# Kernel optimization log

Hardware: AMD Instinct MI355X
Metric: run time of the kernel (lower is better)

The kernel has to match this reference:

```python
import jax, jax.numpy as jnp
import numpy as np

N = 50000
E = 800000
D_IN, D_HID, D_OUT = 256, 512, 256
LN_EPS = 1e-5


def setup_inputs() -> dict:
    key = jax.random.key(0)
    ks = jax.random.split(key, 8)
    return {
        "v": jax.random.normal(ks[0], (N, D_IN), dtype=jnp.float32),
        "edge_weight": jax.random.uniform(ks[1], (E,), dtype=jnp.float32),
        "epsilon": jnp.zeros((1, 1), dtype=jnp.float32),
        "w1": jax.random.normal(ks[2], (D_HID, D_IN), dtype=jnp.float32) * (1.0 / np.sqrt(D_IN)),
        "b1": jnp.zeros((D_HID,), dtype=jnp.float32),
        "g1": jnp.ones((D_HID,), dtype=jnp.float32),
        "beta1": jnp.zeros((D_HID,), dtype=jnp.float32),
        "w2": jax.random.normal(ks[3], (D_OUT, D_HID), dtype=jnp.float32) * (1.0 / np.sqrt(D_HID)),
        "b2": jnp.zeros((D_OUT,), dtype=jnp.float32),
        "g2": jnp.ones((D_OUT,), dtype=jnp.float32),
        "beta2": jnp.zeros((D_OUT,), dtype=jnp.float32),
        "src": jax.random.randint(ks[4], (E,), 0, N, dtype=jnp.int32),
        "dst": jax.random.randint(ks[5], (E,), 0, N, dtype=jnp.int32),
    }


def _layer_norm(x, g, b):
    mu = jnp.mean(x, axis=-1, keepdims=True)
    var = jnp.mean(jnp.square(x - mu), axis=-1, keepdims=True)
    return (x - mu) * jax.lax.rsqrt(var + LN_EPS) * g + b


def reference(v, edge_weight, epsilon, w1, b1, g1, beta1, w2, b2, g2, beta2, src, dst):
    # sparse adjacency aggregation: agg[dst] += w * v[src]   (torch.sparse.mm(a, v))
    msgs = v[src] * edge_weight[:, None]            # [E, D_IN]
    agg = jax.ops.segment_sum(msgs, dst, num_segments=v.shape[0])  # [N, D_IN]
    h = agg + epsilon * v                            # epsilon residual
    # MLP: Linear -> LayerNorm -> ReLU  (x2)
    h = jax.nn.relu(_layer_norm(h @ w1.T + b1, g1, beta1))
    h = jax.nn.relu(_layer_norm(h @ w2.T + b2, g2, beta2))
    return h
```

## Files before the change

kernel.cpp:

```cpp
#include <hip/hip_runtime.h>

#define D_IN 256
#define D_HID 512
#define D_OUT 256
#define LN_EPS 1e-5f
#define SCAN_B 512

typedef __attribute__((ext_vector_type(8))) short bf16x8;
typedef __attribute__((ext_vector_type(4))) float f32x4;

__device__ __forceinline__ ushort f2bf(float x) {
    union { float f; unsigned u; } c; c.f = x;
    unsigned r = c.u + 0x7FFFu + ((c.u >> 16) & 1u);
    return (ushort)(r >> 16);
}
__device__ __forceinline__ float bf2f(unsigned b) {
    union { unsigned u; float f; } c; c.u = b << 16;
    return c.f;
}

__global__ void zero_kernel(int* __restrict__ p, int n) {
    int i = blockIdx.x * 256 + threadIdx.x;
    if (i < n) p[i] = 0;
}

__global__ void hist_kernel(const int* __restrict__ dst, int* __restrict__ cnt, int E) {
    int e = blockIdx.x * 256 + threadIdx.x;
    if (e < E) atomicAdd(&cnt[dst[e]], 1);
}

__global__ __launch_bounds__(SCAN_B) void scan1_kernel(const int* __restrict__ cnt,
                                                       int* __restrict__ offs,
                                                       int* __restrict__ bsum, int n) {
    __shared__ int s[SCAN_B];
    int i = blockIdx.x * SCAN_B + threadIdx.x;
    int x = (i < n) ? cnt[i] : 0;
    s[threadIdx.x] = x;
    __syncthreads();
    for (int o = 1; o < SCAN_B; o <<= 1) {
        int t = (threadIdx.x >= (unsigned)o) ? s[threadIdx.x - o] : 0;
        __syncthreads();
        s[threadIdx.x] += t;
        __syncthreads();
    }
    if (i < n) offs[i] = s[threadIdx.x] - x;
    if (threadIdx.x == SCAN_B - 1) bsum[blockIdx.x] = s[threadIdx.x];
}

__global__ __launch_bounds__(128) void scan2_kernel(int* __restrict__ bsum, int nb) {
    __shared__ int s[128];
    int x = (threadIdx.x < (unsigned)nb) ? bsum[threadIdx.x] : 0;
    s[threadIdx.x] = x;
    __syncthreads();
    for (int o = 1; o < 128; o <<= 1) {
        int t = (threadIdx.x >= (unsigned)o) ? s[threadIdx.x - o] : 0;
        __syncthreads();
        s[threadIdx.x] += t;
        __syncthreads();
    }
    if (threadIdx.x < (unsigned)nb) bsum[threadIdx.x] = s[threadIdx.x] - x;
}

__global__ __launch_bounds__(SCAN_B) void scan3_kernel(int* __restrict__ offs,
                                                       int* __restrict__ cursor,
                                                       const int* __restrict__ bsum,
                                                       int n, int E) {
    int i = blockIdx.x * SCAN_B + threadIdx.x;
    if (i < n) {
        int v0 = offs[i] + bsum[blockIdx.x];
        offs[i] = v0;
        cursor[i] = v0;
    }
    if (i == 0) offs[n] = E;
}

__global__ void fill_kernel(const int* __restrict__ src, const int* __restrict__ dst,
                            const float* __restrict__ ew, int* __restrict__ cursor,
                            int2* __restrict__ perm, int E) {
    int e = blockIdx.x * 256 + threadIdx.x;
    if (e >= E) return;
    int p = atomicAdd(&cursor[dst[e]], 1);
    perm[p] = make_int2(src[e], __float_as_int(ew[e]));
}

__global__ void cvt_bf16_kernel(const float* __restrict__ in, ushort* __restrict__ out, int n4) {
    int i = blockIdx.x * 256 + threadIdx.x;
    if (i >= n4) return;
    float4 x = ((const float4*)in)[i];
    ((ushort4*)out)[i] = make_ushort4(f2bf(x.x), f2bf(x.y), f2bf(x.z), f2bf(x.w));
}

__global__ void cvt_w_kernel(const float* __restrict__ w1, const float* __restrict__ w2,
                             ushort* __restrict__ w1b, ushort* __restrict__ w2b) {
    int i = blockIdx.x * 256 + threadIdx.x;
    const float* src; ushort* dst; int j;
    if (i < 32768) { src = w1; dst = w1b; j = i; }
    else           { src = w2; dst = w2b; j = i - 32768; }
    float4 x = ((const float4*)src)[j];
    ((ushort4*)dst)[j] = make_ushort4(f2bf(x.x), f2bf(x.y), f2bf(x.z), f2bf(x.w));
}

__global__ __launch_bounds__(256) void aggregate_kernel(
    const ushort* __restrict__ vb, const float* __restrict__ eps_p,
    const int* __restrict__ offs, const int2* __restrict__ perm,
    ushort* __restrict__ aggb, int N) {
    int node = blockIdx.x * 4 + (threadIdx.x >> 6);
    if (node >= N) return;
    int lane = threadIdx.x & 63;
    int beg = offs[node], end = offs[node + 1];
    float a0 = 0.f, a1 = 0.f, a2 = 0.f, a3 = 0.f;

    int i = beg;
    for (; i + 4 <= end; i += 4) {
        int2 p0 = perm[i + 0], p1 = perm[i + 1], p2 = perm[i + 2], p3 = perm[i + 3];
        float w0 = __int_as_float(p0.y), w1 = __int_as_float(p1.y);
        float w2 = __int_as_float(p2.y), w3 = __int_as_float(p3.y);
        ushort4 r0 = ((const ushort4*)(vb + (size_t)p0.x * D_IN))[lane];
        ushort4 r1 = ((const ushort4*)(vb + (size_t)p1.x * D_IN))[lane];
        ushort4 r2 = ((const ushort4*)(vb + (size_t)p2.x * D_IN))[lane];
        ushort4 r3 = ((const ushort4*)(vb + (size_t)p3.x * D_IN))[lane];
        a0 += w0 * bf2f(r0.x) + w1 * bf2f(r1.x) + w2 * bf2f(r2.x) + w3 * bf2f(r3.x);
        a1 += w0 * bf2f(r0.y) + w1 * bf2f(r1.y) + w2 * bf2f(r2.y) + w3 * bf2f(r3.y);
        a2 += w0 * bf2f(r0.z) + w1 * bf2f(r1.z) + w2 * bf2f(r2.z) + w3 * bf2f(r3.z);
        a3 += w0 * bf2f(r0.w) + w1 * bf2f(r1.w) + w2 * bf2f(r2.w) + w3 * bf2f(r3.w);
    }
    for (; i < end; ++i) {
        int2 p = perm[i];
        float w = __int_as_float(p.y);
        ushort4 r = ((const ushort4*)(vb + (size_t)p.x * D_IN))[lane];
        a0 += w * bf2f(r.x); a1 += w * bf2f(r.y);
        a2 += w * bf2f(r.z); a3 += w * bf2f(r.w);
    }
    float eps = eps_p[0];
    ushort4 m = ((const ushort4*)(vb + (size_t)node * D_IN))[lane];
    a0 += eps * bf2f(m.x); a1 += eps * bf2f(m.y);
    a2 += eps * bf2f(m.z); a3 += eps * bf2f(m.w);
    ((ushort4*)(aggb + (size_t)node * D_IN))[lane] =
        make_ushort4(f2bf(a0), f2bf(a1), f2bf(a2), f2bf(a3));
}

template <int COLS, int WRITE_BF16>
__global__ __launch_bounds__(256) void gemm_ln_kernel(
    const ushort* __restrict__ A, const ushort* __restrict__ B,
    const float* __restrict__ bias, const float* __restrict__ g,
    const float* __restrict__ beta, void* __restrict__ Cv, int M, int K) {
    constexpr int CW = COLS / 4;
    constexpr int CF = CW / 16;
    __shared__ ushort As[32 * 32];
    __shared__ ushort Bs[COLS * 32];
    __shared__ float red[2][32][4];
    __shared__ float mu_s[32], rs_s[32];

    int t = threadIdx.x;
    int w = t >> 6, lane = t & 63;
    int row0 = blockIdx.x * 32;
    int fr = lane & 15, q = lane >> 4, kb = q * 8;
    int lrow = lane >> 2;
    int lcol = (lane & 3) * 8;

    f32x4 acc[2][CF];
    #pragma unroll
    for (int i = 0; i < 2; ++i)
        #pragma unroll
        for (int c = 0; c < CF; ++c) {
            f32x4 z = {0.f, 0.f, 0.f, 0.f};
            acc[i][c] = z;
        }

    for (int k0 = 0; k0 < K; k0 += 32) {
        #pragma unroll
        for (int c = 0; c < CF; ++c) {
            int br = w * CW + c * 16 + lrow;
            const ushort* gp = B + (size_t)br * K + k0 + lcol;
            __builtin_amdgcn_global_load_lds(
                (const __attribute__((address_space(1))) void*)gp,
                (__attribute__((address_space(3))) void*)(&Bs[(w * CW + c * 16) * 32]),
                16, 0, 0);
        }
        if (w < 2) {
            int ar = row0 + w * 16 + lrow;
            if (ar > M - 1) ar = M - 1;
            const ushort* gp = A + (size_t)ar * K + k0 + lcol;
            __builtin_amdgcn_global_load_lds(
                (const __attribute__((address_space(1))) void*)gp,
                (__attribute__((address_space(3))) void*)(&As[(w * 16) * 32]),
                16, 0, 0);
        }
        __syncthreads();

        bf16x8 af[2], bf[CF];
        af[0] = *(const bf16x8*)&As[fr * 32 + kb];
        af[1] = *(const bf16x8*)&As[(16 + fr) * 32 + kb];
        #pragma unroll
        for (int c = 0; c < CF; ++c)
            bf[c] = *(const bf16x8*)&Bs[(w * CW + c * 16 + fr) * 32 + kb];
        #pragma unroll
        for (int i = 0; i < 2; ++i)
            #pragma unroll
            for (int c = 0; c < CF; ++c)
                acc[i][c] = __builtin_amdgcn_mfma_f32_16x16x32_bf16(af[i], bf[c], acc[i][c], 0, 0, 0);
        __syncthreads();
    }

    float bi[CF], gg[CF], bb[CF];
    #pragma unroll
    for (int c = 0; c < CF; ++c) {
        int col = w * CW + c * 16 + fr;
        bi[c] = bias[col]; gg[c] = g[col]; bb[c] = beta[col];
    }

    #pragma unroll
    for (int i = 0; i < 2; ++i) {
        #pragma unroll
        for (int r = 0; r < 4; ++r) {
            float s = 0.f, sq = 0.f;
            #pragma unroll
            for (int c = 0; c < CF; ++c) {
                float x = acc[i][c][r] + bi[c];
                acc[i][c][r] = x;
                s += x; sq += x * x;
            }
            #pragma unroll
            for (int o = 1; o < 16; o <<= 1) {
                s  += __shfl_xor(s, o, 64);
                sq += __shfl_xor(sq, o, 64);
            }
            if (fr == 0) {
                int row = i * 16 + q * 4 + r;
                red[0][row][w] = s;
                red[1][row][w] = sq;
            }
        }
    }
    __syncthreads();
    if (t < 32) {
        float s  = red[0][t][0] + red[0][t][1] + red[0][t][2] + red[0][t][3];
        float sq = red[1][t][0] + red[1][t][1] + red[1][t][2] + red[1][t][3];
        float mu = s / (float)COLS;
        float var = sq / (float)COLS - mu * mu;
        mu_s[t] = mu;
        rs_s[t] = rsqrtf(var + LN_EPS);
    }
    __syncthreads();

    #pragma unroll
    for (int i = 0; i < 2; ++i) {
        #pragma unroll
        for (int r = 0; r < 4; ++r) {
            int row = i * 16 + q * 4 + r;
            int grow = row0 + row;
            if (grow >= M) continue;
            float mu = mu_s[row], rs = rs_s[row];
            #pragma unroll
            for (int c = 0; c < CF; ++c) {
                int col = w * CW + c * 16 + fr;
                float y = (acc[i][c][r] - mu) * rs * gg[c] + bb[c];
                y = fmaxf(y, 0.f);
                if (WRITE_BF16)
                    ((ushort*)Cv)[(size_t)grow * COLS + col] = f2bf(y);
                else
                    ((float*)Cv)[(size_t)grow * COLS + col] = y;
            }
        }
    }
}

extern "C" void kernel_launch(void* const* d_in, const int* in_sizes, int n_in,
                              void* d_out, int out_size, void* d_ws, size_t ws_size,
                              hipStream_t stream) {
    const float* v     = (const float*)d_in[0];
    const float* ew    = (const float*)d_in[1];
    const float* eps   = (const float*)d_in[2];
    const float* w1    = (const float*)d_in[3];
    const float* b1    = (const float*)d_in[4];
    const float* g1    = (const float*)d_in[5];
    const float* beta1 = (const float*)d_in[6];
    const float* w2    = (const float*)d_in[7];
    const float* b2    = (const float*)d_in[8];
    const float* g2    = (const float*)d_in[9];
    const float* beta2 = (const float*)d_in[10];
    const int*   src   = (const int*)d_in[11];
    const int*   dst   = (const int*)d_in[12];

    int N = in_sizes[0] / D_IN;
    int E = in_sizes[1];

    float* out = (float*)d_out;

    char* ws = (char*)d_ws;
    size_t off = 0;
    ushort* vb   = (ushort*)(ws + off); off += (size_t)N * D_IN * 2;
    ushort* aggb = (ushort*)(ws + off); off += (size_t)N * D_IN * 2;
    ushort* h1b  = (ushort*)(ws + off); off += (size_t)N * D_HID * 2;
    ushort* w1b  = (ushort*)(ws + off); off += (size_t)D_HID * D_IN * 2;
    ushort* w2b  = (ushort*)(ws + off); off += (size_t)D_OUT * D_HID * 2;
    int* offs     = (int*)(ws + off); off += (size_t)(N + 256) * 4;
    int* cursor   = (int*)(ws + off); off += (size_t)(N + 256) * 4;
    int* bsum     = (int*)(ws + off); off += 1024;
    int2* perm    = (int2*)(ws + off); off += (size_t)E * 8;

    int nb = (N + SCAN_B - 1) / SCAN_B;

    zero_kernel<<<(N + 255) / 256, 256, 0, stream>>>(cursor, N);
    hist_kernel<<<(E + 255) / 256, 256, 0, stream>>>(dst, cursor, E);
    scan1_kernel<<<nb, SCAN_B, 0, stream>>>(cursor, offs, bsum, N);
    scan2_kernel<<<1, 128, 0, stream>>>(bsum, nb);
    scan3_kernel<<<nb, SCAN_B, 0, stream>>>(offs, cursor, bsum, N, E);
    fill_kernel<<<(E + 255) / 256, 256, 0, stream>>>(src, dst, ew, cursor, perm, E);

    cvt_bf16_kernel<<<((size_t)N * D_IN / 4 + 255) / 256, 256, 0, stream>>>(v, vb, N * D_IN / 4);
    cvt_w_kernel<<<256, 256, 0, stream>>>(w1, w2, w1b, w2b);

    aggregate_kernel<<<(N + 3) / 4, 256, 0, stream>>>(vb, eps, offs, perm, aggb, N);

    int mblocks = (N + 31) / 32;
    gemm_ln_kernel<D_HID, 1><<<mblocks, 256, 0, stream>>>(
        aggb, w1b, b1, g1, beta1, h1b, N, D_IN);

    gemm_ln_kernel<D_OUT, 0><<<mblocks, 256, 0, stream>>>(
        h1b, w2b, b2, g2, beta2, out, N, D_HID);
}
```

Before: 363.7 us.

## Fuse aggregation and both GEMM+LayerNorm layers into one kernel, merge prep launches

New measurement: 421.7 us. 1.16x slower.

```diff
diff --git a/kernel.cpp b/kernel.cpp
--- a/kernel.cpp
+++ b/kernel.cpp
@@ -19,9 +19,32 @@
     return c.f;
 }
 
-__global__ void zero_kernel(int* __restrict__ p, int n) {
-    int i = blockIdx.x * 256 + threadIdx.x;
-    if (i < n) p[i] = 0;
+__global__ void prep_kernel(const float* __restrict__ v, const float* __restrict__ w1,
+                            const float* __restrict__ w2, ushort* __restrict__ vb,
+                            ushort* __restrict__ w1b, ushort* __restrict__ w2b,
+                            int* __restrict__ cnt, int n4v, int nzero,
+                            int bv, int bw) {
+    int b = blockIdx.x, t = threadIdx.x;
+    if (b < bv) {
+        int i = b * 256 + t;
+        if (i < n4v) {
+            float4 x = ((const float4*)v)[i];
+            ((ushort4*)vb)[i] = make_ushort4(f2bf(x.x), f2bf(x.y), f2bf(x.z), f2bf(x.w));
+        }
+    } else if (b < bv + bw) {
+        int j = (b - bv) * 256 + t;
+        if (j < 32768) {
+            float4 x = ((const float4*)w1)[j];
+            ((ushort4*)w1b)[j] = make_ushort4(f2bf(x.x), f2bf(x.y), f2bf(x.z), f2bf(x.w));
+        } else {
+            int k = j - 32768;
+            float4 x = ((const float4*)w2)[k];
+            ((ushort4*)w2b)[k] = make_ushort4(f2bf(x.x), f2bf(x.y), f2bf(x.z), f2bf(x.w));
+        }
+    } else {
+        int i = (b - bv - bw) * 256 + t;
+        if (i < nzero) cnt[i] = 0;
+    }
 }
 
 __global__ void hist_kernel(const int* __restrict__ dst, int* __restrict__ cnt, int E) {
@@ -47,27 +70,22 @@
     if (threadIdx.x == SCAN_B - 1) bsum[blockIdx.x] = s[threadIdx.x];
 }
 
-__global__ __launch_bounds__(128) void scan2_kernel(int* __restrict__ bsum, int nb) {
-    __shared__ int s[128];
-    int x = (threadIdx.x < (unsigned)nb) ? bsum[threadIdx.x] : 0;
-    s[threadIdx.x] = x;
-    __syncthreads();
-    for (int o = 1; o < 128; o <<= 1) {
-        int t = (threadIdx.x >= (unsigned)o) ? s[threadIdx.x - o] : 0;
-        __syncthreads();
-        s[threadIdx.x] += t;
-        __syncthreads();
-    }
-    if (threadIdx.x < (unsigned)nb) bsum[threadIdx.x] = s[threadIdx.x] - x;
-}
-
 __global__ __launch_bounds__(SCAN_B) void scan3_kernel(int* __restrict__ offs,
                                                        int* __restrict__ cursor,
                                                        const int* __restrict__ bsum,
-                                                       int n, int E) {
-    int i = blockIdx.x * SCAN_B + threadIdx.x;
+                                                       int n, int E, int nb) {
+    __shared__ int s[SCAN_B];
+    int t = threadIdx.x;
+    s[t] = (t < nb && t < (int)blockIdx.x) ? bsum[t] : 0;
+    __syncthreads();
+    for (int o = SCAN_B / 2; o > 0; o >>= 1) {
+        if (t < o) s[t] += s[t + o];
+        __syncthreads();
+    }
+    int base = s[0];
+    int i = blockIdx.x * SCAN_B + t;
     if (i < n) {
-        int v0 = offs[i] + bsum[blockIdx.x];
+        int v0 = offs[i] + base;
         offs[i] = v0;
         cursor[i] = v0;
     }
@@ -83,71 +101,19 @@
     perm[p] = make_int2(src[e], __float_as_int(ew[e]));
 }
 
-__global__ void cvt_bf16_kernel(const float* __restrict__ in, ushort* __restrict__ out, int n4) {
-    int i = blockIdx.x * 256 + threadIdx.x;
-    if (i >= n4) return;
-    float4 x = ((const float4*)in)[i];
-    ((ushort4*)out)[i] = make_ushort4(f2bf(x.x), f2bf(x.y), f2bf(x.z), f2bf(x.w));
-}
-
-__global__ void cvt_w_kernel(const float* __restrict__ w1, const float* __restrict__ w2,
-                             ushort* __restrict__ w1b, ushort* __restrict__ w2b) {
-    int i = blockIdx.x * 256 + threadIdx.x;
-    const float* src; ushort* dst; int j;
-    if (i < 32768) { src = w1; dst = w1b; j = i; }
-    else           { src = w2; dst = w2b; j = i - 32768; }
-    float4 x = ((const float4*)src)[j];
-    ((ushort4*)dst)[j] = make_ushort4(f2bf(x.x), f2bf(x.y), f2bf(x.z), f2bf(x.w));
-}
-
-__global__ __launch_bounds__(256) void aggregate_kernel(
+#define ASTR 264
+#define HSTR 520
+#define BS1_OFF 8448
+#define BS2_OFF 16640
+
+__global__ __launch_bounds__(256) void mega_kernel(
     const ushort* __restrict__ vb, const float* __restrict__ eps_p,
     const int* __restrict__ offs, const int2* __restrict__ perm,
-    ushort* __restrict__ aggb, int N) {
-    int node = blockIdx.x * 4 + (threadIdx.x >> 6);
-    if (node >= N) return;
-    int lane = threadIdx.x & 63;
-    int beg = offs[node], end = offs[node + 1];
-    float a0 = 0.f, a1 = 0.f, a2 = 0.f, a3 = 0.f;
-
-    int i = beg;
-    for (; i + 4 <= end; i += 4) {
-        int2 p0 = perm[i + 0], p1 = perm[i + 1], p2 = perm[i + 2], p3 = perm[i + 3];
-        float w0 = __int_as_float(p0.y), w1 = __int_as_float(p1.y);
-        float w2 = __int_as_float(p2.y), w3 = __int_as_float(p3.y);
-        ushort4 r0 = ((const ushort4*)(vb + (size_t)p0.x * D_IN))[lane];
-        ushort4 r1 = ((const ushort4*)(vb + (size_t)p1.x * D_IN))[lane];
-        ushort4 r2 = ((const ushort4*)(vb + (size_t)p2.x * D_IN))[lane];
-        ushort4 r3 = ((const ushort4*)(vb + (size_t)p3.x * D_IN))[lane];
-        a0 += w0 * bf2f(r0.x) + w1 * bf2f(r1.x) + w2 * bf2f(r2.x) + w3 * bf2f(r3.x);
-        a1 += w0 * bf2f(r0.y) + w1 * bf2f(r1.y) + w2 * bf2f(r2.y) + w3 * bf2f(r3.y);
-        a2 += w0 * bf2f(r0.z) + w1 * bf2f(r1.z) + w2 * bf2f(r2.z) + w3 * bf2f(r3.z);
-        a3 += w0 * bf2f(r0.w) + w1 * bf2f(r1.w) + w2 * bf2f(r2.w) + w3 * bf2f(r3.w);
-    }
-    for (; i < end; ++i) {
-        int2 p = perm[i];
-        float w = __int_as_float(p.y);
-        ushort4 r = ((const ushort4*)(vb + (size_t)p.x * D_IN))[lane];
-        a0 += w * bf2f(r.x); a1 += w * bf2f(r.y);
-        a2 += w * bf2f(r.z); a3 += w * bf2f(r.w);
-    }
-    float eps = eps_p[0];
-    ushort4 m = ((const ushort4*)(vb + (size_t)node * D_IN))[lane];
-    a0 += eps * bf2f(m.x); a1 += eps * bf2f(m.y);
-    a2 += eps * bf2f(m.z); a3 += eps * bf2f(m.w);
-    ((ushort4*)(aggb + (size_t)node * D_IN))[lane] =
-        make_ushort4(f2bf(a0), f2bf(a1), f2bf(a2), f2bf(a3));
-}
-
-template <int COLS, int WRITE_BF16>
-__global__ __launch_bounds__(256) void gemm_ln_kernel(
-    const ushort* __restrict__ A, const ushort* __restrict__ B,
-    const float* __restrict__ bias, const float* __restrict__ g,
-    const float* __restrict__ beta, void* __restrict__ Cv, int M, int K) {
-    constexpr int CW = COLS / 4;
-    constexpr int CF = CW / 16;
-    __shared__ ushort As[32 * 32];
-    __shared__ ushort Bs[COLS * 32];
+    const ushort* __restrict__ w1b, const ushort* __restrict__ w2b,
+    const float* __restrict__ b1, const float* __restrict__ g1, const float* __restrict__ be1,
+    const float* __restrict__ b2, const float* __restrict__ g2, const float* __restrict__ be2,
+    float* __restrict__ out, int N) {
+    __shared__ ushort lds[24832];
     __shared__ float red[2][32][4];
     __shared__ float mu_s[32], rs_s[32];
 
@@ -155,111 +121,226 @@
     int w = t >> 6, lane = t & 63;
     int row0 = blockIdx.x * 32;
     int fr = lane & 15, q = lane >> 4, kb = q * 8;
-    int lrow = lane >> 2;
-    int lcol = (lane & 3) * 8;
-
-    f32x4 acc[2][CF];
+    int lrow = lane >> 2, lcol = (lane & 3) * 8;
+
+    float epsv = eps_p[0];
+    for (int s = 0; s < 8; ++s) {
+        int lnode = w * 8 + s;
+        int node = row0 + lnode;
+        float a0 = 0.f, a1 = 0.f, a2 = 0.f, a3 = 0.f;
+        if (node < N) {
+            int beg = offs[node], end = offs[node + 1];
+            int i = beg;
+            for (; i + 4 <= end; i += 4) {
+                int2 p0 = perm[i + 0], p1 = perm[i + 1], p2 = perm[i + 2], p3 = perm[i + 3];
+                float w0 = __int_as_float(p0.y), w1f = __int_as_float(p1.y);
+                float w2f = __int_as_float(p2.y), w3 = __int_as_float(p3.y);
+                ushort4 r0 = ((const ushort4*)(vb + (size_t)p0.x * D_IN))[lane];
+                ushort4 r1 = ((const ushort4*)(vb + (size_t)p1.x * D_IN))[lane];
+                ushort4 r2 = ((const ushort4*)(vb + (size_t)p2.x * D_IN))[lane];
+                ushort4 r3 = ((const ushort4*)(vb + (size_t)p3.x * D_IN))[lane];
+                a0 += w0 * bf2f(r0.x) + w1f * bf2f(r1.x) + w2f * bf2f(r2.x) + w3 * bf2f(r3.x);
+                a1 += w0 * bf2f(r0.y) + w1f * bf2f(r1.y) + w2f * bf2f(r2.y) + w3 * bf2f(r3.y);
+                a2 += w0 * bf2f(r0.z) + w1f * bf2f(r1.z) + w2f * bf2f(r2.z) + w3 * bf2f(r3.z);
+                a3 += w0 * bf2f(r0.w) + w1f * bf2f(r1.w) + w2f * bf2f(r2.w) + w3 * bf2f(r3.w);
+            }
+            for (; i < end; ++i) {
+                int2 p = perm[i];
+                float wf = __int_as_float(p.y);
+                ushort4 r = ((const ushort4*)(vb + (size_t)p.x * D_IN))[lane];
+                a0 += wf * bf2f(r.x); a1 += wf * bf2f(r.y);
+                a2 += wf * bf2f(r.z); a3 += wf * bf2f(r.w);
+            }
+            ushort4 m = ((const ushort4*)(vb + (size_t)node * D_IN))[lane];
+            a0 += epsv * bf2f(m.x); a1 += epsv * bf2f(m.y);
+            a2 += epsv * bf2f(m.z); a3 += epsv * bf2f(m.w);
+        }
+        uint2 pk;
+        pk.x = (unsigned)f2bf(a0) | ((unsigned)f2bf(a1) << 16);
+        pk.y = (unsigned)f2bf(a2) | ((unsigned)f2bf(a3) << 16);
+        *(uint2*)&lds[lnode * ASTR + lane * 4] = pk;
+    }
+    __syncthreads();
+
+    f32x4 acc[2][8];
     #pragma unroll
     for (int i = 0; i < 2; ++i)
         #pragma unroll
-        for (int c = 0; c < CF; ++c) {
+        for (int c = 0; c < 8; ++c) {
             f32x4 z = {0.f, 0.f, 0.f, 0.f};
             acc[i][c] = z;
         }
 
-    for (int k0 = 0; k0 < K; k0 += 32) {
-        #pragma unroll
-        for (int c = 0; c < CF; ++c) {
-            int br = w * CW + c * 16 + lrow;
-            const ushort* gp = B + (size_t)br * K + k0 + lcol;
+    for (int k0 = 0; k0 < D_IN; k0 += 32) {
+        #pragma unroll
+        for (int c = 0; c < 8; ++c) {
+            int br = w * 128 + c * 16 + lrow;
+            const ushort* gp = w1b + (size_t)br * D_IN + k0 + lcol;
             __builtin_amdgcn_global_load_lds(
                 (const __attribute__((address_space(1))) void*)gp,
-                (__attribute__((address_space(3))) void*)(&Bs[(w * CW + c * 16) * 32]),
+                (__attribute__((address_space(3))) void*)(&lds[BS1_OFF + (w * 128 + c * 16) * 32]),
                 16, 0, 0);
         }
-        if (w < 2) {
-            int ar = row0 + w * 16 + lrow;
-            if (ar > M - 1) ar = M - 1;
-            const ushort* gp = A + (size_t)ar * K + k0 + lcol;
+        __syncthreads();
+        bf16x8 af[2], bf[8];
+        af[0] = *(const bf16x8*)&lds[fr * ASTR + k0 + kb];
+        af[1] = *(const bf16x8*)&lds[(16 + fr) * ASTR + k0 + kb];
+        #pragma unroll
+        for (int c = 0; c < 8; ++c)
+            bf[c] = *(const bf16x8*)&lds[BS1_OFF + (w * 128 + c * 16 + fr) * 32 + kb];
+        #pragma unroll
+        for (int i = 0; i < 2; ++i)
+            #pragma unroll
+            for (int c = 0; c < 8; ++c)
+                acc[i][c] = __builtin_amdgcn_mfma_f32_16x16x32_bf16(af[i], bf[c], acc[i][c], 0, 0, 0);
+        __syncthreads();
+    }
+
+    {
+        float bi[8], gg[8], bb[8];
+        #pragma unroll
+        for (int c = 0; c < 8; ++c) {
+            int col = w * 128 + c * 16 + fr;
+            bi[c] = b1[col]; gg[c] = g1[col]; bb[c] = be1[col];
+        }
+        #pragma unroll
+        for (int i = 0; i < 2; ++i) {
+            #pragma unroll
+            for (int r = 0; r < 4; ++r) {
+                float s = 0.f, sq = 0.f;
+                #pragma unroll
+                for (int c = 0; c < 8; ++c) {
+                    float x = acc[i][c][r] + bi[c];
+                    acc[i][c][r] = x;
+                    s += x; sq += x * x;
+                }
+                #pragma unroll
+                for (int o = 1; o < 16; o <<= 1) {
+                    s  += __shfl_xor(s, o, 64);
+                    sq += __shfl_xor(sq, o, 64);
+                }
+                if (fr == 0) {
+                    int row = i * 16 + q * 4 + r;
+                    red[0][row][w] = s;
+                    red[1][row][w] = sq;
+                }
+            }
+        }
+        __syncthreads();
+        if (t < 32) {
+            float s  = red[0][t][0] + red[0][t][1] + red[0][t][2] + red[0][t][3];
+            float sq = red[1][t][0] + red[1][t][1] + red[1][t][2] + red[1][t][3];
+            float mu = s / (float)D_HID;
+            float var = sq / (float)D_HID - mu * mu;
+            mu_s[t] = mu;
+            rs_s[t] = rsqrtf(var + LN_EPS);
+        }
+        __syncthreads();
+        #pragma unroll
+        for (int i = 0; i < 2; ++i) {
+            #pragma unroll
+            for (int r = 0; r < 4; ++r) {
+                int row = i * 16 + q * 4 + r;
+                float mu = mu_s[row], rs = rs_s[row];
+                #pragma unroll
+                for (int c = 0; c < 8; ++c) {
+                    int col = w * 128 + c * 16 + fr;
+                    float y = (acc[i][c][r] - mu) * rs * gg[c] + bb[c];
+                    lds[row * HSTR + col] = f2bf(fmaxf(y, 0.f));
+                }
+            }
+        }
+    }
+    __syncthreads();
+
+    f32x4 acc2[2][4];
+    #pragma unroll
+    for (int i = 0; i < 2; ++i)
+        #pragma unroll
+        for (int c = 0; c < 4; ++c) {
+            f32x4 z = {0.f, 0.f, 0.f, 0.f};
+            acc2[i][c] = z;
+        }
+
+    for (int k0 = 0; k0 < D_HID; k0 += 32) {
+        #pragma unroll
+        for (int c = 0; c < 4; ++c) {
+            int br = w * 64 + c * 16 + lrow;
+            const ushort* gp = w2b + (size_t)br * D_HID + k0 + lcol;
             __builtin_amdgcn_global_load_lds(
                 (const __attribute__((address_space(1))) void*)gp,
-                (__attribute__((address_space(3))) void*)(&As[(w * 16) * 32]),
+                (__attribute__((address_space(3))) void*)(&lds[BS2_OFF + (w * 64 + c * 16) * 32]),
                 16, 0, 0);
         }
         __syncthreads();
-
-        bf16x8 af[2], bf[CF];
-        af[0] = *(const bf16x8*)&As[fr * 32 + kb];
-        af[1] = *(const bf16x8*)&As[(16 + fr) * 32 + kb];
-        #pragma unroll
-        for (int c = 0; c < CF; ++c)
-            bf[c] = *(const bf16x8*)&Bs[(w * CW + c * 16 + fr) * 32 + kb];
+        bf16x8 af[2], bf[4];
+        af[0] = *(const bf16x8*)&lds[fr * HSTR + k0 + kb];
+        af[1] = *(const bf16x8*)&lds[(16 + fr) * HSTR + k0 + kb];
+        #pragma unroll
+        for (int c = 0; c < 4; ++c)
+            bf[c] = *(const bf16x8*)&lds[BS2_OFF + (w * 64 + c * 16 + fr) * 32 + kb];
         #pragma unroll
         for (int i = 0; i < 2; ++i)
             #pragma unroll
-            for (int c = 0; c < CF; ++c)
-                acc[i][c] = __builtin_amdgcn_mfma_f32_16x16x32_bf16(af[i], bf[c], acc[i][c], 0, 0, 0);
-        __syncthreads();
-    }
-
-    float bi[CF], gg[CF], bb[CF];
-    #pragma unroll
-    for (int c = 0; c < CF; ++c) {
-        int col = w * CW + c * 16 + fr;
-        bi[c] = bias[col]; gg[c] = g[col]; bb[c] = beta[col];
-    }
-
-    #pragma unroll
-    for (int i = 0; i < 2; ++i) {
-        #pragma unroll
-        for (int r = 0; r < 4; ++r) {
-            float s = 0.f, sq = 0.f;
-            #pragma unroll
-            for (int c = 0; c < CF; ++c) {
-                float x = acc[i][c][r] + bi[c];
-                acc[i][c][r] = x;
-                s += x; sq += x * x;
-            }
-            #pragma unroll
-            for (int o = 1; o < 16; o <<= 1) {
-                s  += __shfl_xor(s, o, 64);
-                sq += __shfl_xor(sq, o, 64);
-            }
-            if (fr == 0) {
+            for (int c = 0; c < 4; ++c)
+                acc2[i][c] = __builtin_amdgcn_mfma_f32_16x16x32_bf16(af[i], bf[c], acc2[i][c], 0, 0, 0);
+        __syncthreads();
+    }
+
+    {
+        float bi[4], gg[4], bb[4];
+        #pragma unroll
+        for (int c = 0; c < 4; ++c) {
+            int col = w * 64 + c * 16 + fr;
+            bi[c] = b2[col]; gg[c] = g2[col]; bb[c] = be2[col];
+        }
+        #pragma unroll
+        for (int i = 0; i < 2; ++i) {
+            #pragma unroll
+            for (int r = 0; r < 4; ++r) {
+                float s = 0.f, sq = 0.f;
+                #pragma unroll
+                for (int c = 0; c < 4; ++c) {
+                    float x = acc2[i][c][r] + bi[c];
+                    acc2[i][c][r] = x;
+                    s += x; sq += x * x;
+                }
+                #pragma unroll
+                for (int o = 1; o < 16; o <<= 1) {
+                    s  += __shfl_xor(s, o, 64);
+                    sq += __shfl_xor(sq, o, 64);
+                }
+                if (fr == 0) {
+                    int row = i * 16 + q * 4 + r;
+                    red[0][row][w] = s;
+                    red[1][row][w] = sq;
+                }
+            }
+        }
+        __syncthreads();
+        if (t < 32) {
+            float s  = red[0][t][0] + red[0][t][1] + red[0][t][2] + red[0][t][3];
+            float sq = red[1][t][0] + red[1][t][1] + red[1][t][2] + red[1][t][3];
+            float mu = s / (float)D_OUT;
+            float var = sq / (float)D_OUT - mu * mu;
+            mu_s[t] = mu;
+            rs_s[t] = rsqrtf(var + LN_EPS);
+        }
+        __syncthreads();
+        #pragma unroll
+        for (int i = 0; i < 2; ++i) {
+            #pragma unroll
+            for (int r = 0; r < 4; ++r) {
                 int row = i * 16 + q * 4 + r;
-                red[0][row][w] = s;
-                red[1][row][w] = sq;
-            }
-        }
-    }
-    __syncthreads();
-    if (t < 32) {
-        float s  = red[0][t][0] + red[0][t][1] + red[0][t][2] + red[0][t][3];
-        float sq = red[1][t][0] + red[1][t][1] + red[1][t][2] + red[1][t][3];
-        float mu = s / (float)COLS;
-        float var = sq / (float)COLS - mu * mu;
-        mu_s[t] = mu;
-        rs_s[t] = rsqrtf(var + LN_EPS);
-    }
-    __syncthreads();
-
-    #pragma unroll
-    for (int i = 0; i < 2; ++i) {
-        #pragma unroll
-        for (int r = 0; r < 4; ++r) {
-            int row = i * 16 + q * 4 + r;
-            int grow = row0 + row;
-            if (grow >= M) continue;
-            float mu = mu_s[row], rs = rs_s[row];
-            #pragma unroll
-            for (int c = 0; c < CF; ++c) {
-                int col = w * CW + c * 16 + fr;
-                float y = (acc[i][c][r] - mu) * rs * gg[c] + bb[c];
-                y = fmaxf(y, 0.f);
-                if (WRITE_BF16)
-                    ((ushort*)Cv)[(size_t)grow * COLS + col] = f2bf(y);
-                else
-                    ((float*)Cv)[(size_t)grow * COLS + col] = y;
+                int grow = row0 + row;
+                if (grow >= N) continue;
+                float mu = mu_s[row], rs = rs_s[row];
+                #pragma unroll
+                for (int c = 0; c < 4; ++c) {
+                    int col = w * 64 + c * 16 + fr;
+                    float y = (acc2[i][c][r] - mu) * rs * gg[c] + bb[c];
+                    out[(size_t)grow * D_OUT + col] = fmaxf(y, 0.f);
+                }
             }
         }
     }
@@ -290,8 +371,6 @@
     char* ws = (char*)d_ws;
     size_t off = 0;
     ushort* vb   = (ushort*)(ws + off); off += (size_t)N * D_IN * 2;
-    ushort* aggb = (ushort*)(ws + off); off += (size_t)N * D_IN * 2;
-    ushort* h1b  = (ushort*)(ws + off); off += (size_t)N * D_HID * 2;
     ushort* w1b  = (ushort*)(ws + off); off += (size_t)D_HID * D_IN * 2;
     ushort* w2b  = (ushort*)(ws + off); off += (size_t)D_OUT * D_HID * 2;
     int* offs     = (int*)(ws + off); off += (size_t)(N + 256) * 4;
@@ -300,23 +379,20 @@
     int2* perm    = (int2*)(ws + off); off += (size_t)E * 8;
 
     int nb = (N + SCAN_B - 1) / SCAN_B;
-
-    zero_kernel<<<(N + 255) / 256, 256, 0, stream>>>(cursor, N);
+    int n4v = N * (D_IN / 4);
+    int bv = (n4v + 255) / 256;
+    int bw = 256;
+    int bz = (N + 255) / 256;
+
+    prep_kernel<<<bv + bw + bz, 256, 0, stream>>>(v, w1, w2, vb, w1b, w2b,
+                                                  cursor, n4v, N, bv, bw);
+
     hist_kernel<<<(E + 255) / 256, 256, 0, stream>>>(dst, cursor, E);
     scan1_kernel<<<nb, SCAN_B, 0, stream>>>(cursor, offs, bsum, N);
-    scan2_kernel<<<1, 128, 0, stream>>>(bsum, nb);
-    scan3_kernel<<<nb, SCAN_B, 0, stream>>>(offs, cursor, bsum, N, E);
+    scan3_kernel<<<nb, SCAN_B, 0, stream>>>(offs, cursor, bsum, N, E, nb);
     fill_kernel<<<(E + 255) / 256, 256, 0, stream>>>(src, dst, ew, cursor, perm, E);
 
-    cvt_bf16_kernel<<<((size_t)N * D_IN / 4 + 255) / 256, 256, 0, stream>>>(v, vb, N * D_IN / 4);
-    cvt_w_kernel<<<256, 256, 0, stream>>>(w1, w2, w1b, w2b);
-
-    aggregate_kernel<<<(N + 3) / 4, 256, 0, stream>>>(vb, eps, offs, perm, aggb, N);
-
     int mblocks = (N + 31) / 32;
-    gemm_ln_kernel<D_HID, 1><<<mblocks, 256, 0, stream>>>(
-        aggb, w1b, b1, g1, beta1, h1b, N, D_IN);
-
-    gemm_ln_kernel<D_OUT, 0><<<mblocks, 256, 0, stream>>>(
-        h1b, w2b, b2, g2, beta2, out, N, D_HID);
-}
+    mega_kernel<<<mblocks, 256, 0, stream>>>(vb, eps, offs, perm, w1b, w2b,
+                                             b1, g1, beta1, b2, g2, beta2, out, N);
+}
```
